# Kernel optimization log

Hardware: AMD Instinct MI355X
Metric: run time of the kernel (lower is better)

The kernel has to match this reference:

```python
import jax, jax.numpy as jnp
import numpy as np

NB = 256  # images are quantized to 256 intensity levels (uint8 pipeline)


def _histograms(q):
    # q: int32 (BC, N) values in [0, NB)
    BC, N = q.shape
    idx = (q + jnp.arange(BC, dtype=jnp.int32)[:, None] * NB).reshape(-1)
    ones = jnp.ones((BC * N,), dtype=jnp.int32)
    return jax.ops.segment_sum(ones, idx, num_segments=BC * NB).reshape(BC, NB)


def _match_lut(counts_s, counts_r):
    # Fixed-shape emulation of the per-channel np.unique/cumsum/np.interp loop.
    occ_s = counts_s > 0
    occ_r = counts_r > 0
    first_s = jnp.argmax(occ_s)  # smallest unique source value (dropped, maps to 0)
    first_r = jnp.argmax(occ_r)  # smallest unique reference value (dropped)
    cs = counts_s.at[first_s].set(0)
    cr = counts_r.at[first_r].set(0)
    cums = jnp.cumsum(cs).astype(jnp.float32)
    cumr = jnp.cumsum(cr).astype(jnp.float32)
    s_q = cums / jnp.maximum(cums[-1], 1.0)  # source quantiles at every bin
    r_q = cumr / jnp.maximum(cumr[-1], 1.0)
    # Compact occupied reference bins (excluding the first) to the front so that
    # jnp.interp sees only the quantiles/values that np.unique would produce.
    occ_r2 = occ_r & (jnp.arange(NB) != first_r)
    order = jnp.argsort(jnp.logical_not(occ_r2))  # stable: occupied bins first, ascending
    occ_sorted = occ_r2[order]
    xp = jnp.where(occ_sorted, r_q[order], 2.0)   # pad with x>1 so queries (<=1) never reach pads
    fp = jnp.where(occ_sorted, order.astype(jnp.float32), 0.0)
    lut = jnp.trunc(jnp.interp(s_q, xp, fp))  # trunc == C-style cast into uint8 result buffer
    lut = lut.at[first_s].set(0.0)            # interp_value[0] = 0 in the original
    ok = (jnp.sum(occ_s) > 1) & (jnp.sum(occ_r) > 1)  # 'continue' branch -> zeros
    return jnp.where(ok, lut, 0.0)


def _match_histogram(source, reference):
    # source/reference: float (B,3,H,W) with values at exact 0..255 levels
    B, C, H, W = source.shape
    sq = jnp.clip(jnp.round(source), 0, NB - 1).astype(jnp.int32).reshape(B * C, H * W)
    rq = jnp.clip(jnp.round(reference), 0, NB - 1).astype(jnp.int32).reshape(B * C, H * W)
    lut = jax.vmap(_match_lut)(_histograms(sq), _histograms(rq))  # (BC, NB)
    return jnp.take_along_axis(lut, sq, axis=1).reshape(B, C, H, W)


def reference(input_data, target_data, ref_data, mask_src, mask_tar):
    to_img = lambda x: (x + 1.0) * 0.5 * 255.0  # tensor2image(x) * 255
    inp = to_img(input_data)
    tar = to_img(target_data)
    ref = to_img(ref_data)
    m_src = jnp.broadcast_to(mask_src, inp.shape)
    m_tar = jnp.broadcast_to(mask_tar, tar.shape)
    input_masked = inp * m_src
    target_masked = tar * m_tar
    ref_masked = ref * m_src
    matched = jax.lax.stop_gradient(_match_histogram(ref_masked, target_masked))
    input_match = matched * m_src
    return jnp.mean(jnp.abs(input_masked - input_match))  # L1Loss


def setup_inputs() -> dict:
    key = jax.random.key(0)
    k1, k2, k3, k4, k5 = jax.random.split(key, 5)
    B, H, W = 8, 512, 512

    def img(k):
        # exact multiples of 1/255 in [-1,1] -> integer 0..255 after tensor2image*255
        levels = jax.random.randint(k, (B, 3, H, W), 0, 256).astype(jnp.float32)
        return (levels / 255.0) * 2.0 - 1.0

    def mask(k):
        return (jax.random.uniform(k, (B, 1, H, W)) > 0.3).astype(jnp.float32)

    return {
        "input_data": img(k1),
        "target_data": img(k2),
        "ref_data": img(k3),
        "mask_src": mask(k4),
        "mask_tar": mask(k5),
    }
```

## Files before the change

kernel.cpp:

```cpp
#include <hip/hip_runtime.h>

#define HW    262144
#define HW4   65536
#define BC    24
#define NB    256
#define NTOT  6291456

#define GH    64
#define GL    64
#define TOTL  (BC * GL)

#define WS_HSP_OFF   0
#define WS_HRP_OFF   1572864
#define WS_LUT_OFF   3145728
#define WS_LSUM_OFF  3170304
#define WS_QM_OFF    3176448

__device__ __forceinline__ int quantize(float x, float m) {
    float v = (x + 1.0f) * 0.5f * 255.0f * m;
    float r = rintf(v);
    r = fminf(fmaxf(r, 0.0f), 255.0f);
    return (int)r;
}

__device__ __forceinline__ int incl_scan256(int v, int t, int* buf4, int* tot) {
    const int lane = t & 63;
    const int wave = t >> 6;
#pragma unroll
    for (int off = 1; off < 64; off <<= 1) {
        int y = __shfl_up(v, off, 64);
        if (lane >= off) v += y;
    }
    __syncthreads();
    if (lane == 63) buf4[wave] = v;
    __syncthreads();
    int add = 0;
#pragma unroll
    for (int w = 0; w < 4; ++w) if (w < wave) add += buf4[w];
    *tot = buf4[0] + buf4[1] + buf4[2] + buf4[3];
    return v + add;
}

__global__ void __launch_bounds__(256)
hist_kernel(const float4* __restrict__ ref4,
            const float4* __restrict__ tar4,
            const float4* __restrict__ ms4,
            const float4* __restrict__ mt4,
            int* __restrict__ hsPart, int* __restrict__ hrPart,
            ushort4* __restrict__ qm) {
    __shared__ int wh[4 * 2 * NB];
    const int t = threadIdx.x;
    const int wave = t >> 6;
    const int lane = t & 63;
#pragma unroll
    for (int j = 0; j < 8; ++j) wh[t + j * 256] = 0;
    __syncthreads();

    const int c = blockIdx.y;
    const int b = c / 3;
    const float4* refc = ref4 + (size_t)c * HW4;
    const float4* tarc = tar4 + (size_t)c * HW4;
    const float4* msb  = ms4 + (size_t)b * HW4;
    const float4* mtb  = mt4 + (size_t)b * HW4;
    ushort4* qmc = qm + (size_t)c * HW4;

    const int base = blockIdx.x * 256 + t;

    float4 R[4], T[4], M[4], MT[4];
#pragma unroll
    for (int j = 0; j < 4; ++j) R[j]  = refc[base + j * 16384];
#pragma unroll
    for (int j = 0; j < 4; ++j) M[j]  = msb[base + j * 16384];
#pragma unroll
    for (int j = 0; j < 4; ++j) T[j]  = tarc[base + j * 16384];
#pragma unroll
    for (int j = 0; j < 4; ++j) MT[j] = mtb[base + j * 16384];

    int* whS = &wh[wave * 512];
    int* whR = &wh[wave * 512 + 256];
    int n0s = 0, n0r = 0;
#pragma unroll
    for (int j = 0; j < 4; ++j) {
        const float rv[4]  = {R[j].x, R[j].y, R[j].z, R[j].w};
        const float mv[4]  = {M[j].x, M[j].y, M[j].z, M[j].w};
        const float tvv[4] = {T[j].x, T[j].y, T[j].z, T[j].w};
        const float mtv[4] = {MT[j].x, MT[j].y, MT[j].z, MT[j].w};
        unsigned u16[4];
#pragma unroll
        for (int k = 0; k < 4; ++k) {
            const int qs = quantize(rv[k], mv[k]);
            const bool ms_on = (mv[k] != 0.0f);
            u16[k] = (unsigned)qs | (ms_on ? 256u : 0u);
            if (ms_on) atomicAdd(&whS[qs], 1);
            else n0s++;
            if (mtv[k] != 0.0f) atomicAdd(&whR[quantize(tvv[k], mtv[k])], 1);
            else n0r++;
        }
        ushort4 qq;
        qq.x = (unsigned short)u16[0];
        qq.y = (unsigned short)u16[1];
        qq.z = (unsigned short)u16[2];
        qq.w = (unsigned short)u16[3];
        qmc[base + j * 16384] = qq;
    }
#pragma unroll
    for (int off = 32; off > 0; off >>= 1) {
        n0s += __shfl_down(n0s, off);
        n0r += __shfl_down(n0r, off);
    }
    if (lane == 0) {
        if (n0s) atomicAdd(&whS[0], n0s);
        if (n0r) atomicAdd(&whR[0], n0r);
    }
    __syncthreads();

    const int s = wh[t] + wh[512 + t] + wh[1024 + t] + wh[1536 + t];
    const int r = wh[256 + t] + wh[768 + t] + wh[1280 + t] + wh[1792 + t];
    hsPart[(c * GH + blockIdx.x) * NB + t] = s;
    hrPart[(c * GH + blockIdx.x) * NB + t] = r;
}

__global__ void __launch_bounds__(256)
lut_kernel(const int* __restrict__ hsPart,
           const int* __restrict__ hrPart,
           float* __restrict__ lut) {
    const int c = blockIdx.x;
    const int t = threadIdx.x;

    __shared__ int   buf4[4];
    __shared__ float xp[NB];
    __shared__ float fp[NB];
    __shared__ int firstS, firstR, nOccS, nOccR;

    int cs = 0, cr = 0;
#pragma unroll 8
    for (int g = 0; g < GH; ++g) {
        cs += hsPart[(c * GH + g) * NB + t];
        cr += hrPart[(c * GH + g) * NB + t];
    }

    if (t == 0) { firstS = NB; firstR = NB; nOccS = 0; nOccR = 0; }
    __syncthreads();
    if (cs > 0) { atomicMin(&firstS, t); atomicAdd(&nOccS, 1); }
    if (cr > 0) { atomicMin(&firstR, t); atomicAdd(&nOccR, 1); }
    __syncthreads();

    const int csz = (t == firstS) ? 0 : cs;
    const int crz = (t == firstR) ? 0 : cr;

    int totS, totR, dummy;
    const int cumS = incl_scan256(csz, t, buf4, &totS);
    const int cumR = incl_scan256(crz, t, buf4, &totR);
    const int occ2 = (cr > 0 && t != firstR) ? 1 : 0;
    const int rank = incl_scan256(occ2, t, buf4, &dummy) - occ2;

    const float x  = (float)cumS / fmaxf((float)totS, 1.0f);
    const float rq = (float)cumR / fmaxf((float)totR, 1.0f);

    xp[t] = 2.0f;
    fp[t] = 0.0f;
    __syncthreads();
    if (occ2) { xp[rank] = rq; fp[rank] = (float)t; }
    __syncthreads();

    int lo = 0, hi = NB;
    while (lo < hi) {
        int mid = (lo + hi) >> 1;
        if (xp[mid] > x) hi = mid; else lo = mid + 1;
    }
    int i2 = lo;
    i2 = (i2 < 1) ? 1 : ((i2 > NB - 1) ? NB - 1 : i2);
    float dxv = xp[i2] - xp[i2 - 1];
    float f;
    if (dxv == 0.0f) f = fp[i2];
    else f = fp[i2 - 1] + (x - xp[i2 - 1]) / dxv * (fp[i2] - fp[i2 - 1]);
    if (x < xp[0]) f = fp[0];

    float l = truncf(f);
    if (t == firstS) l = 0.0f;
    if (!((nOccS > 1) && (nOccR > 1))) l = 0.0f;

    lut[c * NB + t] = l;
}

__global__ void __launch_bounds__(256)
loss_kernel(const float4* __restrict__ inp4,
            const ushort4* __restrict__ qm,
            const float* __restrict__ lut,
            float* __restrict__ lsum) {
    __shared__ float llut[NB];
    __shared__ float wsum[4];
    const int t = threadIdx.x;
    const int c = blockIdx.y;
    const int g = blockIdx.x;
    const int lane = t & 63;
    const int wave = t >> 6;

    const float4*  inpc = inp4 + (size_t)c * HW4;
    const ushort4* qmc  = qm + (size_t)c * HW4;
    const int base = g * 256 + t;

    float4  X[4];
    ushort4 Q[4];
#pragma unroll
    for (int j = 0; j < 4; ++j) X[j] = inpc[base + j * 16384];
#pragma unroll
    for (int j = 0; j < 4; ++j) Q[j] = qmc[base + j * 16384];

    llut[t] = lut[c * NB + t];
    __syncthreads();

    float s = 0.0f;
#pragma unroll
    for (int j = 0; j < 4; ++j) {
        const float xv[4] = {X[j].x, X[j].y, X[j].z, X[j].w};
        const unsigned qv[4] = {Q[j].x, Q[j].y, Q[j].z, Q[j].w};
#pragma unroll
        for (int k = 0; k < 4; ++k) {
            const int q = (int)(qv[k] & 255u);
            const float mf = (float)((qv[k] >> 8) & 1u);
            const float im = (xv[k] + 1.0f) * 127.5f;
            s += mf * fabsf(im - llut[q]);
        }
    }

#pragma unroll
    for (int off = 32; off > 0; off >>= 1) s += __shfl_down(s, off);
    if (lane == 0) wsum[wave] = s;
    __syncthreads();
    if (t == 0)
        lsum[c * GL + g] = wsum[0] + wsum[1] + wsum[2] + wsum[3];
}

__global__ void __launch_bounds__(256)
finalize_kernel(const float* __restrict__ lsum, float* __restrict__ out) {
    const int t = threadIdx.x;
    float s = 0.0f;
#pragma unroll
    for (int i = t; i < TOTL; i += 256) s += lsum[i];
#pragma unroll
    for (int off = 32; off > 0; off >>= 1) s += __shfl_down(s, off);
    __shared__ float wsum[4];
    const int lane = t & 63;
    const int wave = t >> 6;
    if (lane == 0) wsum[wave] = s;
    __syncthreads();
    if (t == 0)
        out[0] = (wsum[0] + wsum[1] + wsum[2] + wsum[3]) / (float)NTOT;
}

extern "C" void kernel_launch(void* const* d_in, const int* in_sizes, int n_in,
                              void* d_out, int out_size, void* d_ws, size_t ws_size,
                              hipStream_t stream) {
    const float* inp  = (const float*)d_in[0];
    const float* tar  = (const float*)d_in[1];
    const float* ref  = (const float*)d_in[2];
    const float* msrc = (const float*)d_in[3];
    const float* mtar = (const float*)d_in[4];

    char* ws = (char*)d_ws;
    int*      hsPart = (int*)(ws + WS_HSP_OFF);
    int*      hrPart = (int*)(ws + WS_HRP_OFF);
    float*    lut    = (float*)(ws + WS_LUT_OFF);
    float*    lsum   = (float*)(ws + WS_LSUM_OFF);
    ushort4*  qm     = (ushort4*)(ws + WS_QM_OFF);

    hist_kernel<<<dim3(GH, BC), 256, 0, stream>>>(
        (const float4*)ref, (const float4*)tar,
        (const float4*)msrc, (const float4*)mtar,
        hsPart, hrPart, qm);

    lut_kernel<<<BC, 256, 0, stream>>>(hsPart, hrPart, lut);

    loss_kernel<<<dim3(GL, BC), 256, 0, stream>>>(
        (const float4*)inp, qm, lut, lsum);

    finalize_kernel<<<1, 256, 0, stream>>>(lsum, (float*)d_out);
}
```

Measured before the change: 132.4 us.

## Pack intermediate quant/mask compactly and fuse final reduction into loss kernel

The 16-bit per-pixel quantized-value-plus-mask intermediate is split into an 8-bit quantized buffer and a 16-bit per-thread mask bitfield, roughly halving intermediate write and read traffic between the histogram and loss kernels. The separate finalize kernel is removed. The last loss block, found through an atomic counter reset in the histogram kernel, now performs the global reduction, saving one launch. This adds atomic traffic and relies on atomic reads for visibility of the partial sums.

```diff
diff --git a/kernel.cpp b/kernel.cpp
--- a/kernel.cpp
+++ b/kernel.cpp
@@ -14,7 +14,9 @@
 #define WS_HRP_OFF   1572864
 #define WS_LUT_OFF   3145728
 #define WS_LSUM_OFF  3170304
-#define WS_QM_OFF    3176448
+#define WS_CNT_OFF   3176448
+#define WS_QB_OFF    3176464
+#define WS_MB_OFF    9467920
 
 __device__ __forceinline__ int quantize(float x, float m) {
     float v = (x + 1.0f) * 0.5f * 255.0f * m;
@@ -47,11 +49,15 @@
             const float4* __restrict__ ms4,
             const float4* __restrict__ mt4,
             int* __restrict__ hsPart, int* __restrict__ hrPart,
-            ushort4* __restrict__ qm) {
+            uchar4* __restrict__ qb, unsigned short* __restrict__ mb,
+            unsigned* __restrict__ finCnt) {
     __shared__ int wh[4 * 2 * NB];
     const int t = threadIdx.x;
     const int wave = t >> 6;
     const int lane = t & 63;
+
+    if (blockIdx.x == 0 && blockIdx.y == 0 && t == 0) *finCnt = 0u;
+
 #pragma unroll
     for (int j = 0; j < 8; ++j) wh[t + j * 256] = 0;
     __syncthreads();
@@ -62,7 +68,8 @@
     const float4* tarc = tar4 + (size_t)c * HW4;
     const float4* msb  = ms4 + (size_t)b * HW4;
     const float4* mtb  = mt4 + (size_t)b * HW4;
-    ushort4* qmc = qm + (size_t)c * HW4;
+    uchar4* qbc = qb + (size_t)c * HW4;
+    unsigned short* mbc = mb + (size_t)c * (GH * 256);
 
     const int base = blockIdx.x * 256 + t;
 
@@ -79,30 +86,32 @@
     int* whS = &wh[wave * 512];
     int* whR = &wh[wave * 512 + 256];
     int n0s = 0, n0r = 0;
+    unsigned mbits = 0u;
 #pragma unroll
     for (int j = 0; j < 4; ++j) {
         const float rv[4]  = {R[j].x, R[j].y, R[j].z, R[j].w};
         const float mv[4]  = {M[j].x, M[j].y, M[j].z, M[j].w};
         const float tvv[4] = {T[j].x, T[j].y, T[j].z, T[j].w};
         const float mtv[4] = {MT[j].x, MT[j].y, MT[j].z, MT[j].w};
-        unsigned u16[4];
+        unsigned q8[4];
 #pragma unroll
         for (int k = 0; k < 4; ++k) {
             const int qs = quantize(rv[k], mv[k]);
-            const bool ms_on = (mv[k] != 0.0f);
-            u16[k] = (unsigned)qs | (ms_on ? 256u : 0u);
-            if (ms_on) atomicAdd(&whS[qs], 1);
+            q8[k] = (unsigned)qs;
+            if (mv[k] != 0.0f) { atomicAdd(&whS[qs], 1); mbits |= 1u << (j * 4 + k); }
             else n0s++;
             if (mtv[k] != 0.0f) atomicAdd(&whR[quantize(tvv[k], mtv[k])], 1);
             else n0r++;
         }
-        ushort4 qq;
-        qq.x = (unsigned short)u16[0];
-        qq.y = (unsigned short)u16[1];
-        qq.z = (unsigned short)u16[2];
-        qq.w = (unsigned short)u16[3];
-        qmc[base + j * 16384] = qq;
-    }
+        uchar4 qq;
+        qq.x = (unsigned char)q8[0];
+        qq.y = (unsigned char)q8[1];
+        qq.z = (unsigned char)q8[2];
+        qq.w = (unsigned char)q8[3];
+        qbc[base + j * 16384] = qq;
+    }
+    mbc[base] = (unsigned short)mbits;
+
 #pragma unroll
     for (int off = 32; off > 0; off >>= 1) {
         n0s += __shfl_down(n0s, off);
@@ -185,27 +194,33 @@
 
 __global__ void __launch_bounds__(256)
 loss_kernel(const float4* __restrict__ inp4,
-            const ushort4* __restrict__ qm,
+            const uchar4* __restrict__ qb,
+            const unsigned short* __restrict__ mb,
             const float* __restrict__ lut,
-            float* __restrict__ lsum) {
+            float* __restrict__ lsum,
+            unsigned* __restrict__ finCnt,
+            float* __restrict__ out) {
     __shared__ float llut[NB];
     __shared__ float wsum[4];
+    __shared__ int isLast;
     const int t = threadIdx.x;
     const int c = blockIdx.y;
     const int g = blockIdx.x;
     const int lane = t & 63;
     const int wave = t >> 6;
 
-    const float4*  inpc = inp4 + (size_t)c * HW4;
-    const ushort4* qmc  = qm + (size_t)c * HW4;
+    const float4* inpc = inp4 + (size_t)c * HW4;
+    const uchar4* qbc  = qb + (size_t)c * HW4;
+    const unsigned short* mbc = mb + (size_t)c * (GL * 256);
     const int base = g * 256 + t;
 
-    float4  X[4];
-    ushort4 Q[4];
+    float4 X[4];
+    uchar4 Q[4];
 #pragma unroll
     for (int j = 0; j < 4; ++j) X[j] = inpc[base + j * 16384];
 #pragma unroll
-    for (int j = 0; j < 4; ++j) Q[j] = qmc[base + j * 16384];
+    for (int j = 0; j < 4; ++j) Q[j] = qbc[base + j * 16384];
+    const unsigned mbits = (unsigned)mbc[base];
 
     llut[t] = lut[c * NB + t];
     __syncthreads();
@@ -217,10 +232,9 @@
         const unsigned qv[4] = {Q[j].x, Q[j].y, Q[j].z, Q[j].w};
 #pragma unroll
         for (int k = 0; k < 4; ++k) {
-            const int q = (int)(qv[k] & 255u);
-            const float mf = (float)((qv[k] >> 8) & 1u);
+            const float mf = (float)((mbits >> (j * 4 + k)) & 1u);
             const float im = (xv[k] + 1.0f) * 127.5f;
-            s += mf * fabsf(im - llut[q]);
+            s += mf * fabsf(im - llut[qv[k]]);
         }
     }
 
@@ -228,25 +242,27 @@
     for (int off = 32; off > 0; off >>= 1) s += __shfl_down(s, off);
     if (lane == 0) wsum[wave] = s;
     __syncthreads();
-    if (t == 0)
-        lsum[c * GL + g] = wsum[0] + wsum[1] + wsum[2] + wsum[3];
-}
-
-__global__ void __launch_bounds__(256)
-finalize_kernel(const float* __restrict__ lsum, float* __restrict__ out) {
-    const int t = threadIdx.x;
-    float s = 0.0f;
-#pragma unroll
-    for (int i = t; i < TOTL; i += 256) s += lsum[i];
-#pragma unroll
-    for (int off = 32; off > 0; off >>= 1) s += __shfl_down(s, off);
-    __shared__ float wsum[4];
-    const int lane = t & 63;
-    const int wave = t >> 6;
-    if (lane == 0) wsum[wave] = s;
-    __syncthreads();
-    if (t == 0)
-        out[0] = (wsum[0] + wsum[1] + wsum[2] + wsum[3]) / (float)NTOT;
+    if (t == 0) {
+        const float blockSum = wsum[0] + wsum[1] + wsum[2] + wsum[3];
+        float old = atomicExch(&lsum[c * GL + g], blockSum);
+        asm volatile("" :: "v"(old) : "memory");
+        unsigned prev = atomicAdd(finCnt, 1u);
+        isLast = (prev == (unsigned)(TOTL - 1)) ? 1 : 0;
+    }
+    __syncthreads();
+
+    if (isLast) {
+        float ss = 0.0f;
+#pragma unroll 2
+        for (int i = t; i < TOTL; i += 256)
+            ss += atomicAdd(&lsum[i], 0.0f);
+#pragma unroll
+        for (int off = 32; off > 0; off >>= 1) ss += __shfl_down(ss, off);
+        if (lane == 0) wsum[wave] = ss;
+        __syncthreads();
+        if (t == 0)
+            out[0] = (wsum[0] + wsum[1] + wsum[2] + wsum[3]) / (float)NTOT;
+    }
 }
 
 extern "C" void kernel_launch(void* const* d_in, const int* in_sizes, int n_in,
@@ -259,21 +275,21 @@
     const float* mtar = (const float*)d_in[4];
 
     char* ws = (char*)d_ws;
-    int*      hsPart = (int*)(ws + WS_HSP_OFF);
-    int*      hrPart = (int*)(ws + WS_HRP_OFF);
-    float*    lut    = (float*)(ws + WS_LUT_OFF);
-    float*    lsum   = (float*)(ws + WS_LSUM_OFF);
-    ushort4*  qm     = (ushort4*)(ws + WS_QM_OFF);
+    int*            hsPart = (int*)(ws + WS_HSP_OFF);
+    int*            hrPart = (int*)(ws + WS_HRP_OFF);
+    float*          lut    = (float*)(ws + WS_LUT_OFF);
+    float*          lsum   = (float*)(ws + WS_LSUM_OFF);
+    unsigned*       finCnt = (unsigned*)(ws + WS_CNT_OFF);
+    uchar4*         qb     = (uchar4*)(ws + WS_QB_OFF);
+    unsigned short* mb     = (unsigned short*)(ws + WS_MB_OFF);
 
     hist_kernel<<<dim3(GH, BC), 256, 0, stream>>>(
         (const float4*)ref, (const float4*)tar,
         (const float4*)msrc, (const float4*)mtar,
-        hsPart, hrPart, qm);
+        hsPart, hrPart, qb, mb, finCnt);
 
     lut_kernel<<<BC, 256, 0, stream>>>(hsPart, hrPart, lut);
 
     loss_kernel<<<dim3(GL, BC), 256, 0, stream>>>(
-        (const float4*)inp, qm, lut, lsum);
-
-    finalize_kernel<<<1, 256, 0, stream>>>(lsum, (float*)d_out);
-}
+        (const float4*)inp, qb, mb, lut, lsum, finCnt, (float*)d_out);
+}
```

Measured after the change: 145.1 us. 9.6% more time.
